# Kernel tuning notes

Hardware: AMD Instinct MI355X
Metric: run time of the kernel (lower is better)

Reference implementation:

```python
import jax, jax.numpy as jnp
import numpy as np

B, C, H, W = 2, 256, 128, 128
GROUPS = 4
BN_EPS = 1e-5


def setup_inputs() -> dict:
    key = jax.random.key(0)
    ks = jax.random.split(key, 8)
    C4 = C // 4
    x = jax.random.normal(ks[0], (B, C, H, W), jnp.float32)
    # deformable offsets: (B, 2*9, H, W), (dy, dx) interleaved per kernel point
    offset = jax.random.normal(ks[1], (B, 18, H, W), jnp.float32) * 1.5
    W0 = jax.random.normal(ks[2], (C4, C), jnp.float32) * 0.01   # conv0 1x1
    b0 = jnp.zeros((C4,), jnp.float32)
    gamma = jnp.ones((C4,), jnp.float32)                          # BatchNorm (eval)
    beta = jnp.zeros((C4,), jnp.float32)
    run_mean = jax.random.normal(ks[3], (C4,), jnp.float32) * 0.1
    run_var = jax.random.uniform(ks[4], (C4,), jnp.float32, 0.5, 1.5)
    W1 = jax.random.normal(ks[5], (GROUPS, C4), jnp.float32) * 0.01  # conv1 1x1
    b1 = jnp.zeros((GROUPS,), jnp.float32)
    return dict(x=x, offset=offset, W0=W0, b0=b0, gamma=gamma, beta=beta,
                run_mean=run_mean, run_var=run_var, W1=W1, b1=b1)


def _deform_unfold_max(x, offset):
    # x: (B,C,H,W); offset: (B,18,H,W) -> max over 9 bilinear samples: (B,C,H,W)
    b, c, h, w = x.shape
    off = offset.reshape(b, 9, 2, h, w)
    ky, kx = jnp.meshgrid(jnp.arange(-1, 2, dtype=x.dtype),
                          jnp.arange(-1, 2, dtype=x.dtype), indexing='ij')
    ky = ky.reshape(9)
    kx = kx.reshape(9)
    yy = jnp.arange(h, dtype=x.dtype)[:, None]
    xx = jnp.arange(w, dtype=x.dtype)[None, :]
    py = yy + ky[:, None, None] + off[:, :, 0]   # (B,9,H,W) sample rows
    px = xx + kx[:, None, None] + off[:, :, 1]   # (B,9,H,W) sample cols
    y0 = jnp.floor(py)
    x0 = jnp.floor(px)
    bidx = jnp.arange(b)[:, None, None, None]
    acc = jnp.zeros((b, 9, h, w, c), x.dtype)
    # bilinear interpolation with zero padding outside the image
    for dy in (0.0, 1.0):
        for dx in (0.0, 1.0):
            yi = y0 + dy
            xi = x0 + dx
            wgt = (1.0 - jnp.abs(py - yi)) * (1.0 - jnp.abs(px - xi))
            valid = (yi >= 0) & (yi <= h - 1) & (xi >= 0) & (xi <= w - 1)
            yc = jnp.clip(yi, 0, h - 1).astype(jnp.int32)
            xc = jnp.clip(xi, 0, w - 1).astype(jnp.int32)
            v = x[bidx, :, yc, xc]               # (B,9,H,W,C) gathered corner
            acc = acc + v * (wgt * valid)[..., None]
    feat = acc.max(axis=1)                        # max over 9 kernel samples
    return feat.transpose(0, 3, 1, 2)             # (B,C,H,W)


def reference(x, offset, W0, b0, gamma, beta, run_mean, run_var, W1, b1):
    feat = _deform_unfold_max(x, offset)
    h = jnp.einsum('bchw,oc->bohw', feat, W0) + b0[:, None, None]
    inv = gamma / jnp.sqrt(run_var + BN_EPS)
    h = (h - run_mean[:, None, None]) * inv[:, None, None] + beta[:, None, None]
    logits = jnp.einsum('bchw,oc->bohw', h, W1) + b1[:, None, None]
    att = jax.nn.sigmoid(logits)                  # (B,groups,H,W)
    reps = x.shape[1] // att.shape[1]
    return jnp.tile(att, (1, reps, 1, 1))         # (B,C,H,W)
```

## Files before the change

kernel.cpp:

```cpp
#include <hip/hip_runtime.h>
#include <math.h>

#define B_   2
#define C_   256
#define C4_  64
#define H_   128
#define W_   128
#define HW_  (H_*W_)
#define G_   4
#define PX_  16
#define NCH_ (W_/PX_)
#define NBLK (B_*H_*NCH_)

__global__ __launch_bounds__(256) void prep_kernel(
    const float* __restrict__ W0, const float* __restrict__ b0,
    const float* __restrict__ gamma, const float* __restrict__ beta,
    const float* __restrict__ rmean, const float* __restrict__ rvar,
    const float* __restrict__ W1, const float* __restrict__ b1,
    float* __restrict__ Weff, float* __restrict__ beff)
{
    __shared__ float inv_s[C4_], shift_s[C4_], wg_s[G_][C4_];
    int t = threadIdx.x;
    if (t < C4_) {
        float inv = gamma[t] * rsqrtf(rvar[t] + 1e-5f);
        inv_s[t]   = inv;
        shift_s[t] = (b0[t] - rmean[t]) * inv + beta[t];
    }
    __syncthreads();
    if (t < G_ * C4_) wg_s[t >> 6][t & 63] = W1[t] * inv_s[t & 63];
    __syncthreads();
    float s0 = 0.f, s1 = 0.f, s2 = 0.f, s3 = 0.f;
    for (int o = 0; o < C4_; ++o) {
        float w0 = W0[o * C_ + t];
        s0 += wg_s[0][o] * w0;
        s1 += wg_s[1][o] * w0;
        s2 += wg_s[2][o] * w0;
        s3 += wg_s[3][o] * w0;
    }
    Weff[0*C_ + t] = s0;
    Weff[1*C_ + t] = s1;
    Weff[2*C_ + t] = s2;
    Weff[3*C_ + t] = s3;
    if (t < G_) {
        float s = b1[t];
        for (int o = 0; o < C4_; ++o) s += W1[t*C4_ + o] * shift_s[o];
        beff[t] = s;
    }
}

__global__ __launch_bounds__(256) void transpose_kernel(
    const float* __restrict__ x, float* __restrict__ xT)
{
    __shared__ float tile[32][33];
    int tx = threadIdx.x, ty = threadIdx.y;
    int hw0 = blockIdx.x * 32, c0 = blockIdx.y * 32, b = blockIdx.z;
    const float* xb  = x  + (size_t)b * C_ * HW_;
    float*       xTb = xT + (size_t)b * C_ * HW_;
    #pragma unroll
    for (int j = 0; j < 4; ++j)
        tile[ty + 8*j][tx] = xb[(size_t)(c0 + ty + 8*j) * HW_ + hw0 + tx];
    __syncthreads();
    #pragma unroll
    for (int j = 0; j < 4; ++j)
        xTb[(size_t)(hw0 + ty + 8*j) * C_ + c0 + tx] = tile[tx][ty + 8*j];
}

template<int FUSED>
__global__ __launch_bounds__(512, 8) void main_kernel(
    const float* __restrict__ xT, const float* __restrict__ offset,
    const float* __restrict__ Weff, const float* __restrict__ beff,
    float* __restrict__ dst)
{
    __shared__ float offs_lds[18][PX_];
    __shared__ float att_lds[G_ * PX_];
    int t = threadIdx.x;
    int wave = t >> 6, lane = t & 63;

    int bid = blockIdx.x;
    int lid = (bid & 7) * (NBLK / 8) + (bid >> 3);
    int xc = lid & (NCH_ - 1);
    int y  = (lid >> 3) & (H_ - 1);
    int b  = lid >> 10;
    int x0 = xc * PX_;
    int c0 = lane * 4;

    const float* xTb  = xT + (size_t)b * HW_ * C_;
    const float* offb = offset + (size_t)b * 18 * HW_ + (size_t)y * W_ + x0;

    if (t < 18 * PX_)
        offs_lds[t >> 4][t & 15] = offb[(size_t)(t >> 4) * HW_ + (t & 15)];

    float wf[G_][4];
    #pragma unroll
    for (int g = 0; g < G_; ++g) {
        float4 v = *(const float4*)(Weff + g*C_ + c0);
        wf[g][0] = v.x; wf[g][1] = v.y; wf[g][2] = v.z; wf[g][3] = v.w;
    }
    float be[G_];
    #pragma unroll
    for (int g = 0; g < G_; ++g) be[g] = beff[g];

    __syncthreads();

    #pragma unroll
    for (int i = 0; i < 2; ++i) {
        int px = wave * 2 + i;
        int x  = x0 + px;
        float fm0 = -3.4028235e38f, fm1 = fm0, fm2 = fm0, fm3 = fm0;

        #pragma unroll
        for (int k = 0; k < 9; ++k) {
            float oy = offs_lds[2*k    ][px];
            float ox = offs_lds[2*k + 1][px];
            float py = (float)(y + (k/3) - 1) + oy;
            float px_ = (float)(x + (k%3) - 1) + ox;
            float y0f = floorf(py), x0f = floorf(px_);
            float fy = py - y0f, fx = px_ - x0f;
            float vy0 = (y0f >=  0.f && y0f <= 127.f) ? 1.f : 0.f;
            float vy1 = (y0f >= -1.f && y0f <= 126.f) ? 1.f : 0.f;
            float vx0 = (x0f >=  0.f && x0f <= 127.f) ? 1.f : 0.f;
            float vx1 = (x0f >= -1.f && x0f <= 126.f) ? 1.f : 0.f;
            float wy0 = (1.f - fy) * vy0, wy1 = fy * vy1;
            float wx0 = (1.f - fx) * vx0, wx1 = fx * vx1;
            int iy0 = min(max((int)y0f,     0), H_-1);
            int iy1 = min(max((int)y0f + 1, 0), H_-1);
            int ix0 = min(max((int)x0f,     0), W_-1);
            int ix1 = min(max((int)x0f + 1, 0), W_-1);
            const float4 v00 = *(const float4*)(xTb + (((size_t)iy0*W_ + ix0) << 8) + c0);
            const float4 v01 = *(const float4*)(xTb + (((size_t)iy0*W_ + ix1) << 8) + c0);
            const float4 v10 = *(const float4*)(xTb + (((size_t)iy1*W_ + ix0) << 8) + c0);
            const float4 v11 = *(const float4*)(xTb + (((size_t)iy1*W_ + ix1) << 8) + c0);
            float w00 = wy0*wx0, w01 = wy0*wx1, w10 = wy1*wx0, w11 = wy1*wx1;
            float a0 = w00*v00.x + w01*v01.x + w10*v10.x + w11*v11.x;
            float a1 = w00*v00.y + w01*v01.y + w10*v10.y + w11*v11.y;
            float a2 = w00*v00.z + w01*v01.z + w10*v10.z + w11*v11.z;
            float a3 = w00*v00.w + w01*v01.w + w10*v10.w + w11*v11.w;
            fm0 = fmaxf(fm0, a0);
            fm1 = fmaxf(fm1, a1);
            fm2 = fmaxf(fm2, a2);
            fm3 = fmaxf(fm3, a3);
        }

        float p[G_];
        #pragma unroll
        for (int g = 0; g < G_; ++g)
            p[g] = wf[g][0]*fm0 + wf[g][1]*fm1 + wf[g][2]*fm2 + wf[g][3]*fm3;

        #pragma unroll
        for (int off2 = 32; off2 > 0; off2 >>= 1) {
            #pragma unroll
            for (int g = 0; g < G_; ++g)
                p[g] += __shfl_xor(p[g], off2);
        }

        if (lane == 0) {
            #pragma unroll
            for (int g = 0; g < G_; ++g)
                att_lds[g*PX_ + px] = 1.f / (1.f + expf(-(p[g] + be[g])));
        }
    }
    __syncthreads();

    if (FUSED) {
        int px = t & 15, cb = t >> 4;
        float* ob = dst + (size_t)b * C_ * HW_ + (size_t)y * W_ + x0;
        #pragma unroll
        for (int cc = 0; cc < 8; ++cc) {
            int c = cb + cc * 32;
            __builtin_nontemporal_store(att_lds[(c & 3) * PX_ + px],
                                        ob + (size_t)c * HW_ + px);
        }
    } else {
        if (t < G_ * PX_) {
            int g = t >> 4, px = t & 15;
            dst[(size_t)(b*G_ + g) * HW_ + (size_t)y * W_ + x0 + px] = att_lds[t];
        }
    }
}

__global__ __launch_bounds__(256) void expand_kernel(
    const float* __restrict__ att, float* __restrict__ out)
{
    int e4 = blockIdx.x * 256 + threadIdx.x;
    int x4 = e4 & 31;
    int y  = (e4 >> 5) & (H_ - 1);
    int c  = (e4 >> 12) & (C_ - 1);
    int b  = (e4 >> 20) & 1;
    float4 v = *(const float4*)(att + ((size_t)(b*G_ + (c & 3)) * HW_) + y*W_ + x4*4);
    *(float4*)(out + ((size_t)(b*C_ + c) * HW_) + y*W_ + x4*4) = v;
}

extern "C" void kernel_launch(void* const* d_in, const int* in_sizes, int n_in,
                              void* d_out, int out_size, void* d_ws, size_t ws_size,
                              hipStream_t stream)
{
    (void)in_sizes; (void)n_in; (void)out_size;
    const float* x      = (const float*)d_in[0];
    const float* offset = (const float*)d_in[1];
    const float* W0     = (const float*)d_in[2];
    const float* b0     = (const float*)d_in[3];
    const float* gamma  = (const float*)d_in[4];
    const float* beta   = (const float*)d_in[5];
    const float* rmean  = (const float*)d_in[6];
    const float* rvar   = (const float*)d_in[7];
    const float* W1     = (const float*)d_in[8];
    const float* b1     = (const float*)d_in[9];
    float* out = (float*)d_out;

    const size_t xT_elems = (size_t)B_ * C_ * HW_;
    const size_t need_fused = (xT_elems + G_*C_ + G_ + 64) * sizeof(float);

    if (ws_size >= need_fused) {
        float* xT   = (float*)d_ws;
        float* Weff = xT + xT_elems;
        float* beff = Weff + G_ * C_;
        prep_kernel<<<dim3(1), dim3(256), 0, stream>>>(
            W0, b0, gamma, beta, rmean, rvar, W1, b1, Weff, beff);
        transpose_kernel<<<dim3(HW_/32, C_/32, B_), dim3(32, 8), 0, stream>>>(x, xT);
        main_kernel<1><<<dim3(NBLK), dim3(512), 0, stream>>>(
            xT, offset, Weff, beff, out);
    } else {
        float* xT   = out;
        float* att  = (float*)d_ws;
        float* Weff = att + (size_t)B_ * G_ * HW_;
        float* beff = Weff + G_ * C_;
        prep_kernel<<<dim3(1), dim3(256), 0, stream>>>(
            W0, b0, gamma, beta, rmean, rvar, W1, b1, Weff, beff);
        transpose_kernel<<<dim3(HW_/32, C_/32, B_), dim3(32, 8), 0, stream>>>(x, xT);
        main_kernel<0><<<dim3(NBLK), dim3(512), 0, stream>>>(
            xT, offset, Weff, beff, att);
        expand_kernel<<<dim3((B_*C_*HW_/4) / 256), dim3(256), 0, stream>>>(att, out);
    }
}
```

Measured before the change: 171.0 us.

## Merge prep into transpose, precompute bilinear taps in LDS, widen pixel tile

Folds the weight-prep kernel into an extra z-slice of the transpose launch, removing one launch. The transpose switches from an LDS tile to register-level float4 4x4 transposes. The main kernel doubles its pixel tile to 32 and precomputes the bilinear weights and byte addresses per (tap, pixel) once into LDS, so they are not recomputed in every wave. The output store is vectorised to float4 nontemporal writes. The larger tile halves the block count and gives each wave more serial work, which risks lower occupancy and latency hiding.

```diff
diff --git a/kernel.cpp b/kernel.cpp
--- a/kernel.cpp
+++ b/kernel.cpp
@@ -8,11 +8,13 @@
 #define W_   128
 #define HW_  (H_*W_)
 #define G_   4
-#define PX_  16
+#define PX_  32
 #define NCH_ (W_/PX_)
 #define NBLK (B_*H_*NCH_)
 
-__global__ __launch_bounds__(256) void prep_kernel(
+typedef float f4_t __attribute__((ext_vector_type(4)));
+
+__device__ void prep_body(
     const float* __restrict__ W0, const float* __restrict__ b0,
     const float* __restrict__ gamma, const float* __restrict__ beta,
     const float* __restrict__ rmean, const float* __restrict__ rvar,
@@ -49,20 +51,39 @@
 }
 
 __global__ __launch_bounds__(256) void transpose_kernel(
-    const float* __restrict__ x, float* __restrict__ xT)
-{
-    __shared__ float tile[32][33];
-    int tx = threadIdx.x, ty = threadIdx.y;
-    int hw0 = blockIdx.x * 32, c0 = blockIdx.y * 32, b = blockIdx.z;
-    const float* xb  = x  + (size_t)b * C_ * HW_;
-    float*       xTb = xT + (size_t)b * C_ * HW_;
-    #pragma unroll
-    for (int j = 0; j < 4; ++j)
-        tile[ty + 8*j][tx] = xb[(size_t)(c0 + ty + 8*j) * HW_ + hw0 + tx];
-    __syncthreads();
-    #pragma unroll
-    for (int j = 0; j < 4; ++j)
-        xTb[(size_t)(hw0 + ty + 8*j) * C_ + c0 + tx] = tile[tx][ty + 8*j];
+    const float* __restrict__ x, float* __restrict__ xT,
+    const float* __restrict__ W0, const float* __restrict__ b0,
+    const float* __restrict__ gamma, const float* __restrict__ beta,
+    const float* __restrict__ rmean, const float* __restrict__ rvar,
+    const float* __restrict__ W1, const float* __restrict__ b1,
+    float* __restrict__ Weff, float* __restrict__ beff)
+{
+    if (blockIdx.z == B_) {
+        if (blockIdx.x == 0 && blockIdx.y == 0)
+            prep_body(W0, b0, gamma, beta, rmean, rvar, W1, b1, Weff, beff);
+        return;
+    }
+    int t = threadIdx.x;
+    int cq  = t & 7;
+    int hw4 = t >> 3;
+    int hw0 = blockIdx.x * 128, c0 = blockIdx.y * 32, b = blockIdx.z;
+
+    const float* xb = x + (size_t)b * C_ * HW_ + (size_t)(c0 + cq*4) * HW_ + hw0 + hw4*4;
+    float4 r0 = *(const float4*)(xb);
+    float4 r1 = *(const float4*)(xb +     HW_);
+    float4 r2 = *(const float4*)(xb + 2 * HW_);
+    float4 r3 = *(const float4*)(xb + 3 * HW_);
+
+    float4 t0 = {r0.x, r1.x, r2.x, r3.x};
+    float4 t1 = {r0.y, r1.y, r2.y, r3.y};
+    float4 t2 = {r0.z, r1.z, r2.z, r3.z};
+    float4 t3 = {r0.w, r1.w, r2.w, r3.w};
+
+    float* xTb = xT + (size_t)b * HW_ * C_ + (size_t)(hw0 + hw4*4) * C_ + c0 + cq*4;
+    *(float4*)(xTb)          = t0;
+    *(float4*)(xTb +     C_) = t1;
+    *(float4*)(xTb + 2 * C_) = t2;
+    *(float4*)(xTb + 3 * C_) = t3;
 }
 
 template<int FUSED>
@@ -71,24 +92,51 @@
     const float* __restrict__ Weff, const float* __restrict__ beff,
     float* __restrict__ dst)
 {
-    __shared__ float offs_lds[18][PX_];
-    __shared__ float att_lds[G_ * PX_];
+    __shared__ float    wgt_lds[9][PX_][4];
+    __shared__ unsigned adr_lds[9][PX_][4];
+    __shared__ float    att_lds[G_][PX_];
+
     int t = threadIdx.x;
     int wave = t >> 6, lane = t & 63;
 
     int bid = blockIdx.x;
     int lid = (bid & 7) * (NBLK / 8) + (bid >> 3);
     int xc = lid & (NCH_ - 1);
-    int y  = (lid >> 3) & (H_ - 1);
-    int b  = lid >> 10;
+    int y  = (lid >> 2) & (H_ - 1);
+    int b  = lid >> 9;
     int x0 = xc * PX_;
     int c0 = lane * 4;
 
-    const float* xTb  = xT + (size_t)b * HW_ * C_;
-    const float* offb = offset + (size_t)b * 18 * HW_ + (size_t)y * W_ + x0;
-
-    if (t < 18 * PX_)
-        offs_lds[t >> 4][t & 15] = offb[(size_t)(t >> 4) * HW_ + (t & 15)];
+    const float* xTb = xT + (size_t)b * HW_ * C_;
+
+    if (t < 9 * PX_) {
+        int k  = t >> 5, px = t & 31;
+        int x  = x0 + px;
+        const float* offb = offset + (size_t)b * 18 * HW_ + (size_t)y * W_;
+        float oy = offb[(size_t)(2*k    ) * HW_ + x];
+        float ox = offb[(size_t)(2*k + 1) * HW_ + x];
+        float py = (float)(y + (k/3) - 1) + oy;
+        float qx = (float)(x + (k%3) - 1) + ox;
+        float y0f = floorf(py), x0f = floorf(qx);
+        float fy = py - y0f, fx = qx - x0f;
+        float vy0 = (y0f >=  0.f && y0f <= 127.f) ? 1.f : 0.f;
+        float vy1 = (y0f >= -1.f && y0f <= 126.f) ? 1.f : 0.f;
+        float vx0 = (x0f >=  0.f && x0f <= 127.f) ? 1.f : 0.f;
+        float vx1 = (x0f >= -1.f && x0f <= 126.f) ? 1.f : 0.f;
+        float wy0 = (1.f - fy) * vy0, wy1 = fy * vy1;
+        float wx0 = (1.f - fx) * vx0, wx1 = fx * vx1;
+        int iy0 = min(max((int)y0f,     0), H_-1);
+        int iy1 = min(max((int)y0f + 1, 0), H_-1);
+        int ix0 = min(max((int)x0f,     0), W_-1);
+        int ix1 = min(max((int)x0f + 1, 0), W_-1);
+        float4 wg = {wy0*wx0, wy0*wx1, wy1*wx0, wy1*wx1};
+        uint4  ad = {(unsigned)((iy0*W_ + ix0) << 10),
+                     (unsigned)((iy0*W_ + ix1) << 10),
+                     (unsigned)((iy1*W_ + ix0) << 10),
+                     (unsigned)((iy1*W_ + ix1) << 10)};
+        *(float4*)(&wgt_lds[k][px][0]) = wg;
+        *(uint4* )(&adr_lds[k][px][0]) = ad;
+    }
 
     float wf[G_][4];
     #pragma unroll
@@ -102,39 +150,26 @@
 
     __syncthreads();
 
+    const char* xTc = (const char*)xTb;
+    int laneoff = lane << 4;
+
     #pragma unroll
-    for (int i = 0; i < 2; ++i) {
-        int px = wave * 2 + i;
-        int x  = x0 + px;
+    for (int i = 0; i < 4; ++i) {
+        int px = wave * 4 + i;
         float fm0 = -3.4028235e38f, fm1 = fm0, fm2 = fm0, fm3 = fm0;
 
         #pragma unroll
         for (int k = 0; k < 9; ++k) {
-            float oy = offs_lds[2*k    ][px];
-            float ox = offs_lds[2*k + 1][px];
-            float py = (float)(y + (k/3) - 1) + oy;
-            float px_ = (float)(x + (k%3) - 1) + ox;
-            float y0f = floorf(py), x0f = floorf(px_);
-            float fy = py - y0f, fx = px_ - x0f;
-            float vy0 = (y0f >=  0.f && y0f <= 127.f) ? 1.f : 0.f;
-            float vy1 = (y0f >= -1.f && y0f <= 126.f) ? 1.f : 0.f;
-            float vx0 = (x0f >=  0.f && x0f <= 127.f) ? 1.f : 0.f;
-            float vx1 = (x0f >= -1.f && x0f <= 126.f) ? 1.f : 0.f;
-            float wy0 = (1.f - fy) * vy0, wy1 = fy * vy1;
-            float wx0 = (1.f - fx) * vx0, wx1 = fx * vx1;
-            int iy0 = min(max((int)y0f,     0), H_-1);
-            int iy1 = min(max((int)y0f + 1, 0), H_-1);
-            int ix0 = min(max((int)x0f,     0), W_-1);
-            int ix1 = min(max((int)x0f + 1, 0), W_-1);
-            const float4 v00 = *(const float4*)(xTb + (((size_t)iy0*W_ + ix0) << 8) + c0);
-            const float4 v01 = *(const float4*)(xTb + (((size_t)iy0*W_ + ix1) << 8) + c0);
-            const float4 v10 = *(const float4*)(xTb + (((size_t)iy1*W_ + ix0) << 8) + c0);
-            const float4 v11 = *(const float4*)(xTb + (((size_t)iy1*W_ + ix1) << 8) + c0);
-            float w00 = wy0*wx0, w01 = wy0*wx1, w10 = wy1*wx0, w11 = wy1*wx1;
-            float a0 = w00*v00.x + w01*v01.x + w10*v10.x + w11*v11.x;
-            float a1 = w00*v00.y + w01*v01.y + w10*v10.y + w11*v11.y;
-            float a2 = w00*v00.z + w01*v01.z + w10*v10.z + w11*v11.z;
-            float a3 = w00*v00.w + w01*v01.w + w10*v10.w + w11*v11.w;
+            float4 wg = *(const float4*)(&wgt_lds[k][px][0]);
+            uint4  ad = *(const uint4* )(&adr_lds[k][px][0]);
+            const float4 v00 = *(const float4*)(xTc + ad.x + laneoff);
+            const float4 v01 = *(const float4*)(xTc + ad.y + laneoff);
+            const float4 v10 = *(const float4*)(xTc + ad.z + laneoff);
+            const float4 v11 = *(const float4*)(xTc + ad.w + laneoff);
+            float a0 = wg.x*v00.x + wg.y*v01.x + wg.z*v10.x + wg.w*v11.x;
+            float a1 = wg.x*v00.y + wg.y*v01.y + wg.z*v10.y + wg.w*v11.y;
+            float a2 = wg.x*v00.z + wg.y*v01.z + wg.z*v10.z + wg.w*v11.z;
+            float a3 = wg.x*v00.w + wg.y*v01.w + wg.z*v10.w + wg.w*v11.w;
             fm0 = fmaxf(fm0, a0);
             fm1 = fmaxf(fm1, a1);
             fm2 = fmaxf(fm2, a2);
@@ -156,24 +191,25 @@
         if (lane == 0) {
             #pragma unroll
             for (int g = 0; g < G_; ++g)
-                att_lds[g*PX_ + px] = 1.f / (1.f + expf(-(p[g] + be[g])));
+                att_lds[g][px] = 1.f / (1.f + expf(-(p[g] + be[g])));
         }
     }
     __syncthreads();
 
     if (FUSED) {
-        int px = t & 15, cb = t >> 4;
         float* ob = dst + (size_t)b * C_ * HW_ + (size_t)y * W_ + x0;
         #pragma unroll
-        for (int cc = 0; cc < 8; ++cc) {
-            int c = cb + cc * 32;
-            __builtin_nontemporal_store(att_lds[(c & 3) * PX_ + px],
-                                        ob + (size_t)c * HW_ + px);
+        for (int rep = 0; rep < 4; ++rep) {
+            int idx = rep * 512 + t;
+            int c   = idx >> 3;
+            int x4  = idx & 7;
+            f4_t v = *(const f4_t*)(&att_lds[c & 3][x4 * 4]);
+            __builtin_nontemporal_store(v, (f4_t*)(ob + (size_t)c * HW_ + x4 * 4));
         }
     } else {
         if (t < G_ * PX_) {
-            int g = t >> 4, px = t & 15;
-            dst[(size_t)(b*G_ + g) * HW_ + (size_t)y * W_ + x0 + px] = att_lds[t];
+            int g = t >> 5, px = t & 31;
+            dst[(size_t)(b*G_ + g) * HW_ + (size_t)y * W_ + x0 + px] = att_lds[g][px];
         }
     }
 }
@@ -214,9 +250,8 @@
         float* xT   = (float*)d_ws;
         float* Weff = xT + xT_elems;
         float* beff = Weff + G_ * C_;
-        prep_kernel<<<dim3(1), dim3(256), 0, stream>>>(
-            W0, b0, gamma, beta, rmean, rvar, W1, b1, Weff, beff);
-        transpose_kernel<<<dim3(HW_/32, C_/32, B_), dim3(32, 8), 0, stream>>>(x, xT);
+        transpose_kernel<<<dim3(HW_/128, C_/32, B_ + 1), dim3(256), 0, stream>>>(
+            x, xT, W0, b0, gamma, beta, rmean, rvar, W1, b1, Weff, beff);
         main_kernel<1><<<dim3(NBLK), dim3(512), 0, stream>>>(
             xT, offset, Weff, beff, out);
     } else {
@@ -224,9 +259,8 @@
         float* att  = (float*)d_ws;
         float* Weff = att + (size_t)B_ * G_ * HW_;
         float* beff = Weff + G_ * C_;
-        prep_kernel<<<dim3(1), dim3(256), 0, stream>>>(
-            W0, b0, gamma, beta, rmean, rvar, W1, b1, Weff, beff);
-        transpose_kernel<<<dim3(HW_/32, C_/32, B_), dim3(32, 8), 0, stream>>>(x, xT);
+        transpose_kernel<<<dim3(HW_/128, C_/32, B_ + 1), dim3(256), 0, stream>>>(
+            x, xT, W0, b0, gamma, beta, rmean, rvar, W1, b1, Weff, beff);
         main_kernel<0><<<dim3(NBLK), dim3(512), 0, stream>>>(
             xT, offset, Weff, beff, att);
         expand_kernel<<<dim3((B_*C_*HW_/4) / 256), dim3(256), 0, stream>>>(att, out);
```

New measurement: 148.8 us. 1.15x faster.
